# Optimization experiments

Measured on AMD Instinct MI355X. Metric: run time of the kernel, lower is better.

Reference implementation:

```python
import jax, jax.numpy as jnp
import numpy as np

B, L, C, H, W = 2, 3, 64, 32, 32
DI, N, DT_RANK, K = 128, 16, 4, 4  # d_inner=2*C, d_state, dt_rank=ceil(C/16), 4 scan dirs


def setup_inputs() -> dict:
    key = jax.random.key(0)
    ks = iter(jax.random.split(key, 48))
    nrm = lambda shape, s=0.02: jax.random.normal(next(ks), shape, jnp.float32) * s
    return {
        "image_sequence": jax.random.normal(next(ks), (B, L, C, H, W), jnp.float32),
        "difficult_zone": jax.random.normal(next(ks), (B, C, H, W), jnp.float32),
        "sigma": jax.random.uniform(next(ks), (B, C, H, W), jnp.float32),
        # LayerNorm2d applied to each frame
        "norm_g": jnp.ones((C,)), "norm_b": jnp.zeros((C,)),
        # ConvolutionalResBlock (in=3C -> out=C), GroupNorm(num_groups=1)
        "gn1_g": jnp.ones((3 * C,)), "gn1_b": jnp.zeros((3 * C,)),
        "conv1_w": nrm((C, 3 * C, 3, 3)), "conv1_b": jnp.zeros((C,)),
        "gn2_g": jnp.ones((C,)), "gn2_b": jnp.zeros((C,)),
        "conv2_w": nrm((C, C, 3, 3)), "conv2_b": jnp.zeros((C,)),
        "skip_w": nrm((C, 3 * C, 1, 1)), "skip_b": jnp.zeros((C,)),
        # VSSBlock pre-norms
        "ln1_g": jnp.ones((C,)), "ln1_b": jnp.zeros((C,)),
        "ln2_g": jnp.ones((C,)), "ln2_b": jnp.zeros((C,)),
        # SS2D
        "in_proj_w": nrm((2 * DI, C)),
        "dwconv_w": nrm((DI, 1, 3, 3)), "dwconv_b": jnp.zeros((DI,)),
        "x_proj_w": nrm((K, DT_RANK + 2 * N, DI)),
        "dt_proj_w": nrm((K, DI, DT_RANK), 0.1),
        "dt_proj_b": jnp.log(jnp.expm1(jnp.full((K, DI), 0.01, jnp.float32))),
        "A_logs": jnp.log(jnp.tile(jnp.arange(1, N + 1, dtype=jnp.float32), (K * DI, 1))),
        "Ds": jnp.ones((K * DI,)),
        "out_norm_g": jnp.ones((DI,)), "out_norm_b": jnp.zeros((DI,)),
        "out_proj_w": nrm((C, DI)),
        # Mlp (hidden = C)
        "fc1_w": nrm((C, C)), "fc1_b": jnp.zeros((C,)),
        "fc2_w": nrm((C, C)), "fc2_b": jnp.zeros((C,)),
    }


def _ln(x, g, b, eps=1e-5):  # layernorm over last axis
    m = x.mean(-1, keepdims=True)
    v = x.var(-1, keepdims=True)
    return (x - m) * jax.lax.rsqrt(v + eps) * g + b


def _ln2d(x, g, b, eps=1e-6):  # per-pixel channel layernorm, NCHW
    m = x.mean(1, keepdims=True)
    v = x.var(1, keepdims=True)
    return (x - m) * jax.lax.rsqrt(v + eps) * g[None, :, None, None] + b[None, :, None, None]


def _gn1(x, g, b, eps=1e-5):  # GroupNorm(num_groups=1), NCHW
    m = x.mean((1, 2, 3), keepdims=True)
    v = x.var((1, 2, 3), keepdims=True)
    return (x - m) * jax.lax.rsqrt(v + eps) * g[None, :, None, None] + b[None, :, None, None]


def _conv(x, w, b, pad):
    y = jax.lax.conv_general_dilated(x, w, (1, 1), [(pad, pad), (pad, pad)],
                                     dimension_numbers=("NCHW", "OIHW", "NCHW"))
    return y + b[None, :, None, None]


def _forward(image_sequence, difficult_zone, sigma, norm_g, norm_b, gn1_g, gn1_b,
             conv1_w, conv1_b, gn2_g, gn2_b, conv2_w, conv2_b, skip_w, skip_b,
             ln1_g, ln1_b, ln2_g, ln2_b, in_proj_w, dwconv_w, dwconv_b, x_proj_w,
             dt_proj_w, dt_proj_b, A_logs, Ds, out_norm_g, out_norm_b, out_proj_w,
             fc1_w, fc1_b, fc2_w, fc2_b):
    b, l, c, h, w = image_sequence.shape
    bl, L2 = b * l, h * w
    # fold frame loop into batch (identical math per frame in the torch loop)
    frames = _ln2d(image_sequence.reshape(bl, c, h, w), norm_g, norm_b)
    dz = jnp.broadcast_to(difficult_zone[:, None], (b, l, c, h, w)).reshape(bl, c, h, w)
    sg = jnp.broadcast_to(sigma[:, None], (b, l, c, h, w)).reshape(bl, c, h, w)
    x = jnp.concatenate([dz, frames, sg], axis=1)  # [bl, 3c, h, w]
    # channel compressor: pre-act conv res block
    hdn = _conv(jax.nn.silu(_gn1(x, gn1_g, gn1_b)), conv1_w, conv1_b, 1)
    hdn = _conv(jax.nn.silu(_gn1(hdn, gn2_g, gn2_b)), conv2_w, conv2_b, 1)
    x = hdn + _conv(x, skip_w, skip_b, 0)          # [bl, c, h, w]
    x = x.transpose(0, 2, 3, 1)                    # [bl, h, w, c]
    # --- VSSBlock (pre-norm): x = x + SS2D(LN(x)) ---
    xn = _ln(x, ln1_g, ln1_b)
    xz = xn @ in_proj_w.T                          # [bl,h,w,2*DI]
    xc, z = jnp.split(xz, 2, axis=-1)
    xc = xc.transpose(0, 3, 1, 2)                  # [bl, DI, h, w]
    xc = jax.lax.conv_general_dilated(xc, dwconv_w, (1, 1), [(1, 1), (1, 1)],
                                      dimension_numbers=("NCHW", "OIHW", "NCHW"),
                                      feature_group_count=DI) + dwconv_b[None, :, None, None]
    xc = jax.nn.silu(xc)
    # 4-direction scan inputs (HW, WH, and their reverses)
    xf = xc.reshape(bl, DI, L2)
    xt = xc.transpose(0, 1, 3, 2).reshape(bl, DI, L2)
    xs = jnp.stack([xf, xt], axis=1)
    xs = jnp.concatenate([xs, jnp.flip(xs, axis=-1)], axis=1)  # [bl, 4, DI, L2]
    x_dbl = jnp.einsum("bkdl,kcd->bkcl", xs, x_proj_w)
    dts, Bs, Cs = jnp.split(x_dbl, [DT_RANK, DT_RANK + N], axis=2)
    dts = jnp.einsum("bkrl,kdr->bkdl", dts, dt_proj_w) + dt_proj_b[None, :, :, None]
    dts = jax.nn.softplus(dts)                     # [bl, 4, DI, L2]
    A = -jnp.exp(A_logs).reshape(K, DI, N)
    dA = jnp.exp(dts[..., None] * A[None, :, :, None, :])            # [bl,4,DI,L2,N]
    dBu = dts[..., None] * Bs.transpose(0, 1, 3, 2)[:, :, None] * xs[..., None]
    a_t = dA.transpose(3, 0, 1, 2, 4)              # [L2, bl, 4, DI, N]
    bu_t = dBu.transpose(3, 0, 1, 2, 4)
    c_t = Cs.transpose(3, 0, 1, 2)                 # [L2, bl, 4, N]

    def step(hid, inp):
        a_i, bu_i, c_i = inp
        hid = a_i * hid + bu_i
        return hid, jnp.einsum("bkdn,bkn->bkd", hid, c_i)

    h0 = jnp.zeros((bl, K, DI, N), xs.dtype)
    _, ys = jax.lax.scan(step, h0, (a_t, bu_t, c_t))                 # [L2, bl, 4, DI]
    ys = ys.transpose(1, 2, 3, 0) + xs * Ds.reshape(K, DI)[None, :, :, None]
    inv = jnp.flip(ys[:, 2:4], axis=-1)
    y = (ys[:, 0] + inv[:, 0]
         + ys[:, 1].reshape(bl, DI, w, h).transpose(0, 1, 3, 2).reshape(bl, DI, L2)
         + inv[:, 1].reshape(bl, DI, w, h).transpose(0, 1, 3, 2).reshape(bl, DI, L2))
    y = _ln(y.transpose(0, 2, 1), out_norm_g, out_norm_b).reshape(bl, h, w, DI)
    y = y * jax.nn.silu(z)
    x = x + y @ out_proj_w.T
    # --- x = x + Mlp(LN(x)) ---
    xn = _ln(x, ln2_g, ln2_b)
    x = x + (jax.nn.gelu(xn @ fc1_w.T + fc1_b, approximate=False) @ fc2_w.T + fc2_b)
    return x.transpose(0, 3, 1, 2).reshape(b, l, c, h, w)


def reference(image_sequence, difficult_zone, sigma, norm_g, norm_b, gn1_g, gn1_b,
              conv1_w, conv1_b, gn2_g, gn2_b, conv2_w, conv2_b, skip_w, skip_b,
              ln1_g, ln1_b, ln2_g, ln2_b, in_proj_w, dwconv_w, dwconv_b, x_proj_w,
              dt_proj_w, dt_proj_b, A_logs, Ds, out_norm_g, out_norm_b, out_proj_w,
              fc1_w, fc1_b, fc2_w, fc2_b):
    return _forward(image_sequence, difficult_zone, sigma, norm_g, norm_b, gn1_g, gn1_b,
                    conv1_w, conv1_b, gn2_g, gn2_b, conv2_w, conv2_b, skip_w, skip_b,
                    ln1_g, ln1_b, ln2_g, ln2_b, in_proj_w, dwconv_w, dwconv_b, x_proj_w,
                    dt_proj_w, dt_proj_b, A_logs, Ds, out_norm_g, out_norm_b, out_proj_w,
                    fc1_w, fc1_b, fc2_w, fc2_b)
```

## Files before the change

### kernel.cpp

```cpp
#include <hip/hip_runtime.h>
#include <math.h>

#define BL    6
#define CCH   64
#define C3    192
#define L2    1024
#define DIC   128
#define NST   16
#define K4    4
#define PSTR  1088
#define NCH   32

#define LOG2E 1.44269504088896340736f
#define LN2C  0.69314718055994530942f

__device__ __forceinline__ float fexp(float x){ return __builtin_amdgcn_exp2f(x*LOG2E); }
__device__ __forceinline__ float fsilu(float x){ return x / (1.f + fexp(-x)); }
__device__ __forceinline__ float fsoftplus(float x){
  if (x > 20.f) return x;
  return __builtin_amdgcn_logf(1.f + fexp(x)) * LN2C;
}
__device__ __forceinline__ float fgelu(float x){
  return 0.5f*x*(1.f + erff(x*0.70710678118654752440f));
}

__global__ __launch_bounds__(256) void k_ln2d(const float* __restrict__ img,
    const float* __restrict__ dz, const float* __restrict__ sg,
    const float* __restrict__ g, const float* __restrict__ b, float* __restrict__ x3c,
    float* __restrict__ psum1, float* __restrict__ psq1){
  __shared__ float ps[4][64], pq[4][64];
  int s = blockIdx.x >> 4;
  int lane = threadIdx.x & 63;
  int cg = threadIdx.x >> 6;
  int p = ((blockIdx.x & 15) << 6) + lane;
  int bsmp = s/3;
  const float* fr = img + (size_t)s*CCH*L2;
  float vals[16]; float sm=0.f, sq=0.f;
  #pragma unroll
  for (int j=0;j<16;++j){
    int c = cg*16+j;
    float v = fr[c*L2+p];
    vals[j]=v; sm+=v; sq+=v*v;
  }
  ps[cg][lane]=sm; pq[cg][lane]=sq;
  __syncthreads();
  sm = ps[0][lane]+ps[1][lane]+ps[2][lane]+ps[3][lane];
  sq = pq[0][lane]+pq[1][lane]+pq[2][lane]+pq[3][lane];
  float mean = sm*(1.f/CCH); float var = sq*(1.f/CCH) - mean*mean;
  float rs = rsqrtf(var + 1e-6f);
  float* o = x3c + (size_t)s*C3*L2;
  const float* dzp = dz + (size_t)bsmp*CCH*L2;
  const float* sgp = sg + (size_t)bsmp*CCH*L2;
  float gsm=0.f, gsq=0.f;
  #pragma unroll
  for (int j=0;j<16;++j){
    int c = cg*16+j;
    float dzv = dzp[c*L2+p];
    float nv  = (vals[j]-mean)*rs*g[c] + b[c];
    float sgv = sgp[c*L2+p];
    o[c*L2+p] = dzv;
    o[(CCH+c)*L2+p] = nv;
    o[(2*CCH+c)*L2+p] = sgv;
    gsm += dzv+nv+sgv; gsq += dzv*dzv+nv*nv+sgv*sgv;
  }
  for (int m=1;m<64;m<<=1){ gsm+=__shfl_xor(gsm,m,64); gsq+=__shfl_xor(gsq,m,64); }
  __syncthreads();
  if (lane==0){ ps[cg][0]=gsm; pq[cg][0]=gsq; }
  __syncthreads();
  if (threadIdx.x==0){
    psum1[blockIdx.x] = ps[0][0]+ps[1][0]+ps[2][0]+ps[3][0];
    psq1 [blockIdx.x] = pq[0][0]+pq[1][0]+pq[2][0]+pq[3][0];
  }
}

__global__ __launch_bounds__(256) void k_gnact_pad(const float* __restrict__ x,
    const float* __restrict__ psum, const float* __restrict__ psq,
    const float* __restrict__ g, const float* __restrict__ b,
    int ch, int parts, float inv_n, float eps, float* __restrict__ out){
  int bx = blockIdx.x;
  int s = bx / ch; int c = bx % ch;
  int tid = threadIdx.x;
  float sm=0.f, sq=0.f;
  for (int i=0;i<parts;++i){ sm += psum[s*parts+i]; sq += psq[s*parts+i]; }
  float mean = sm*inv_n;
  float var = sq*inv_n - mean*mean;
  float rs = rsqrtf(var + eps);
  float gc = g[c]*rs; float bc = b[c] - mean*rs*g[c];
  float4 v = *(const float4*)(x + (size_t)bx*1024 + tid*4);
  float4 o; o.x = fsilu(v.x*gc+bc); o.y = fsilu(v.y*gc+bc);
  o.z = fsilu(v.z*gc+bc); o.w = fsilu(v.w*gc+bc);
  float* pl = out + (size_t)bx*PSTR;
  *(float4*)(pl + 32 + tid*4) = o;
  float4 z4 = make_float4(0.f,0.f,0.f,0.f);
  if (tid < 8)  *(float4*)(pl + tid*4) = z4;
  else if (tid < 16) *(float4*)(pl + 1056 + (tid-8)*4) = z4;
}

__device__ __forceinline__ void conv_row_acc(float4& a0, float4& a1, float4 mid, float lf, float rt,
    const float* wp0, const float* wp1){
  float w0=wp0[0], w1=wp0[1], w2=wp0[2];
  a0.x = fmaf(w0,lf,   fmaf(w1,mid.x, fmaf(w2,mid.y, a0.x)));
  a0.y = fmaf(w0,mid.x,fmaf(w1,mid.y, fmaf(w2,mid.z, a0.y)));
  a0.z = fmaf(w0,mid.y,fmaf(w1,mid.z, fmaf(w2,mid.w, a0.z)));
  a0.w = fmaf(w0,mid.z,fmaf(w1,mid.w, fmaf(w2,rt,    a0.w)));
  float v0=wp1[0], v1=wp1[1], v2=wp1[2];
  a1.x = fmaf(v0,lf,   fmaf(v1,mid.x, fmaf(v2,mid.y, a1.x)));
  a1.y = fmaf(v0,mid.x,fmaf(v1,mid.y, fmaf(v2,mid.z, a1.y)));
  a1.z = fmaf(v0,mid.y,fmaf(v1,mid.z, fmaf(v2,mid.w, a1.z)));
  a1.w = fmaf(v0,mid.z,fmaf(v1,mid.w, fmaf(v2,rt,    a1.w)));
}

__device__ __forceinline__ void conv_ci_body(float4 m0, float4 m1, float4 m2, int q,
    const float* wp0, const float* wp1, float4& a0, float4& a1){
  float lf0=__shfl_up(m0.w,1,64), rt0=__shfl_down(m0.x,1,64);
  float lf1=__shfl_up(m1.w,1,64), rt1=__shfl_down(m1.x,1,64);
  float lf2=__shfl_up(m2.w,1,64), rt2=__shfl_down(m2.x,1,64);
  if (q==0){ lf0=0.f; lf1=0.f; lf2=0.f; }
  if (q==7){ rt0=0.f; rt1=0.f; rt2=0.f; }
  conv_row_acc(a0,a1,m0,lf0,rt0, wp0+0, wp1+0);
  conv_row_acc(a0,a1,m1,lf1,rt1, wp0+3, wp1+3);
  conv_row_acc(a0,a1,m2,lf2,rt2, wp0+6, wp1+6);
}

__global__ __launch_bounds__(256) void k_conv1_split(const float* __restrict__ xact,
    const float* __restrict__ w, float* __restrict__ part){
  int bx = blockIdx.x; int kk = bx&7; int cop=(bx>>3)&31; int s=bx>>8;
  int co0 = cop*2, co1 = co0+1;
  int tid = threadIdx.x; int row = tid>>3; int q = tid&7; int col0 = q*4;
  float4 a0 = make_float4(0.f,0.f,0.f,0.f);
  float4 a1 = make_float4(0.f,0.f,0.f,0.f);
  int ci0 = kk*24;
  const float* pl = xact + ((size_t)s*C3 + ci0)*PSTR + row*32 + col0;
  const float* wp0 = w + (size_t)(co0*C3 + ci0)*9;
  const float* wp1 = w + (size_t)(co1*C3 + ci0)*9;
  float4 m0 = *(const float4*)(pl);
  float4 m1 = *(const float4*)(pl+32);
  float4 m2 = *(const float4*)(pl+64);
  #pragma unroll 2
  for (int i=0;i<24;++i){
    const float* pn = pl + (i<23 ? PSTR : 0);
    float4 n0 = *(const float4*)(pn);
    float4 n1 = *(const float4*)(pn+32);
    float4 n2 = *(const float4*)(pn+64);
    conv_ci_body(m0,m1,m2,q, wp0, wp1, a0, a1);
    wp0 += 9; wp1 += 9; pl = pn; m0=n0; m1=n1; m2=n2;
  }
  float* pp = part + (size_t)kk*(BL*CCH*L2) + ((size_t)s*CCH+co0)*L2 + row*32+col0;
  *(float4*)pp = a0;
  *(float4*)(pp+L2) = a1;
}

__global__ __launch_bounds__(256) void k_reduce1(const float* __restrict__ part,
    const float* __restrict__ bias, float* __restrict__ h1,
    float* __restrict__ psum2, float* __restrict__ psq2){
  int co = blockIdx.x & 63; int s = blockIdx.x >> 6;
  size_t ofs = ((size_t)s*CCH+co)*L2 + threadIdx.x*4;
  const size_t stride = (size_t)BL*CCH*L2;
  float4 acc = *(const float4*)(part + ofs);
  #pragma unroll
  for (int kk=1;kk<8;++kk){
    float4 r = *(const float4*)(part + (size_t)kk*stride + ofs);
    acc.x += r.x; acc.y += r.y; acc.z += r.z; acc.w += r.w;
  }
  float bv = bias[co];
  acc.x += bv; acc.y += bv; acc.z += bv; acc.w += bv;
  *(float4*)(h1 + ofs) = acc;
  float sm = acc.x+acc.y+acc.z+acc.w;
  float sq = acc.x*acc.x+acc.y*acc.y+acc.z*acc.z+acc.w*acc.w;
  for (int m=1;m<64;m<<=1){ sm+=__shfl_xor(sm,m,64); sq+=__shfl_xor(sq,m,64); }
  __shared__ float s_sm[4], s_sq[4];
  int wv = threadIdx.x>>6;
  if ((threadIdx.x&63)==0){ s_sm[wv]=sm; s_sq[wv]=sq; }
  __syncthreads();
  if (threadIdx.x==0){
    psum2[blockIdx.x] = s_sm[0]+s_sm[1]+s_sm[2]+s_sm[3];
    psq2 [blockIdx.x] = s_sq[0]+s_sq[1]+s_sq[2]+s_sq[3];
  }
}

__global__ __launch_bounds__(256) void k_conv2_split(const float* __restrict__ xact2,
    const float* __restrict__ x3c, const float* __restrict__ w2,
    const float* __restrict__ wsk, float* __restrict__ part){
  int t = blockIdx.x; int role = t % 3; t /= 3;
  int cop = t & 31; int s = t >> 5;
  int co0 = cop*2, co1 = co0+1;
  int tid = threadIdx.x; int row = tid>>3; int q = tid&7; int col0 = q*4;
  int p = row*32+col0;
  float4 a0 = make_float4(0.f,0.f,0.f,0.f);
  float4 a1 = make_float4(0.f,0.f,0.f,0.f);
  if (role < 2){
    int ci0 = role*32;
    const float* pl = xact2 + ((size_t)s*CCH + ci0)*PSTR + row*32 + col0;
    const float* wp0 = w2 + (size_t)(co0*CCH + ci0)*9;
    const float* wp1 = w2 + (size_t)(co1*CCH + ci0)*9;
    float4 m0 = *(const float4*)(pl);
    float4 m1 = *(const float4*)(pl+32);
    float4 m2 = *(const float4*)(pl+64);
    #pragma unroll 2
    for (int i=0;i<32;++i){
      const float* pn = pl + (i<31 ? PSTR : 0);
      float4 n0 = *(const float4*)(pn);
      float4 n1 = *(const float4*)(pn+32);
      float4 n2 = *(const float4*)(pn+64);
      conv_ci_body(m0,m1,m2,q, wp0, wp1, a0, a1);
      wp0 += 9; wp1 += 9; pl = pn; m0=n0; m1=n1; m2=n2;
    }
  } else {
    const float* x3 = x3c + (size_t)s*C3*L2 + p;
    #pragma unroll 4
    for (int ci=0; ci<C3; ++ci){
      float4 v = *(const float4*)(x3 + (size_t)ci*L2);
      float ws0 = wsk[co0*C3+ci], ws1 = wsk[co1*C3+ci];
      a0.x = fmaf(ws0,v.x,a0.x); a0.y = fmaf(ws0,v.y,a0.y); a0.z = fmaf(ws0,v.z,a0.z); a0.w = fmaf(ws0,v.w,a0.w);
      a1.x = fmaf(ws1,v.x,a1.x); a1.y = fmaf(ws1,v.y,a1.y); a1.z = fmaf(ws1,v.z,a1.z); a1.w = fmaf(ws1,v.w,a1.w);
    }
  }
  float* pp = part + (size_t)role*(BL*CCH*L2) + ((size_t)s*CCH+co0)*L2 + p;
  *(float4*)pp = a0;
  *(float4*)(pp+L2) = a1;
}

__global__ __launch_bounds__(256) void k_reduce2(const float* __restrict__ part,
    const float* __restrict__ b2, const float* __restrict__ bsk,
    float* __restrict__ xp, float* __restrict__ x_cmaj){
  int co = blockIdx.x & 63; int s = blockIdx.x >> 6;
  int p = threadIdx.x*4;
  size_t ofs = ((size_t)s*CCH+co)*L2 + p;
  const size_t stride = (size_t)BL*CCH*L2;
  float4 r0 = *(const float4*)(part + ofs);
  float4 r1 = *(const float4*)(part + stride + ofs);
  float4 r2 = *(const float4*)(part + 2*stride + ofs);
  float bv = b2[co]+bsk[co];
  float4 o;
  o.x = r0.x+r1.x+r2.x+bv;
  o.y = r0.y+r1.y+r2.y+bv;
  o.z = r0.z+r1.z+r2.z+bv;
  o.w = r0.w+r1.w+r2.w+bv;
  *(float4*)(x_cmaj + ofs) = o;
  float* xpb = xp + ((size_t)s*L2 + p)*CCH + co;
  xpb[0] = o.x; xpb[CCH] = o.y; xpb[2*CCH] = o.z; xpb[3*CCH] = o.w;
}

__global__ __launch_bounds__(256) void k_ln1_inproj(const float* __restrict__ xp,
    const float* __restrict__ g, const float* __restrict__ b, const float* __restrict__ W,
    float* __restrict__ xc, float* __restrict__ z_t){
  __shared__ float xn_s[64*65];
  int bx = blockIdx.x; int oq = bx & 3; int pg = (bx>>2)&15; int s = bx>>6;
  int p0 = pg*64;
  int tid = threadIdx.x; int wv = __builtin_amdgcn_readfirstlane(tid>>6); int lane = tid&63;
  for (int j=0;j<16;++j){
    int pl = wv*16 + j; int p = p0 + pl;
    float v = xp[((size_t)s*L2 + p)*CCH + lane];
    float sm = v, sq = v*v;
    for (int m=1;m<64;m<<=1){ sm += __shfl_xor(sm,m,64); sq += __shfl_xor(sq,m,64); }
    float mean = sm*(1.f/64.f); float var = sq*(1.f/64.f) - mean*mean;
    float rs = rsqrtf(var + 1e-5f);
    xn_s[pl*65 + lane] = (v-mean)*rs*g[lane] + b[lane];
  }
  __syncthreads();
  int px_l = tid & 63;
  int og = __builtin_amdgcn_readfirstlane(tid >> 6);
  int o0 = oq*64 + og*16;
  float acc[16];
  #pragma unroll
  for (int oi=0;oi<16;++oi) acc[oi]=0.f;
  for (int c=0;c<64;++c){
    float xv = xn_s[px_l*65 + c];
    #pragma unroll
    for (int oi=0;oi<16;++oi) acc[oi] = fmaf(W[(o0+oi)*64 + c], xv, acc[oi]);
  }
  int p = p0 + px_l;
  if (oq < 2){
    #pragma unroll
    for (int oi=0;oi<16;++oi) xc[((size_t)s*DIC + o0 + oi)*L2 + p] = acc[oi];
  } else {
    #pragma unroll
    for (int oi=0;oi<16;++oi) z_t[((size_t)s*DIC + (o0-128) + oi)*L2 + p] = acc[oi];
  }
}

__global__ __launch_bounds__(256) void k_dwconv(const float* __restrict__ xc,
    const float* __restrict__ w, const float* __restrict__ bias, float* __restrict__ xconv){
  int bx = blockIdx.x; int dch = bx & 127; int s = bx >> 7;
  int tid = threadIdx.x; int row = tid>>3; int q = tid&7; int col0 = q*4;
  const float* xr = xc + ((size_t)s*DIC+dch)*L2;
  const float* wp = w + dch*9;
  float bv = bias[dch];
  float4 acc = make_float4(bv,bv,bv,bv);
  #pragma unroll
  for (int dy=-1;dy<=1;++dy){
    int r = row+dy;
    float4 mid = make_float4(0.f,0.f,0.f,0.f);
    if (0<=r && r<32) mid = *(const float4*)(xr + r*32 + col0);
    float lf = __shfl_up(mid.w,1,64); if(q==0) lf=0.f;
    float rt = __shfl_down(mid.x,1,64); if(q==7) rt=0.f;
    float w0=wp[(dy+1)*3], w1=wp[(dy+1)*3+1], w2=wp[(dy+1)*3+2];
    acc.x = fmaf(w0,lf,   fmaf(w1,mid.x, fmaf(w2,mid.y, acc.x)));
    acc.y = fmaf(w0,mid.x,fmaf(w1,mid.y, fmaf(w2,mid.z, acc.y)));
    acc.z = fmaf(w0,mid.y,fmaf(w1,mid.z, fmaf(w2,mid.w, acc.z)));
    acc.w = fmaf(w0,mid.z,fmaf(w1,mid.w, fmaf(w2,rt,    acc.w)));
  }
  acc.x = fsilu(acc.x); acc.y = fsilu(acc.y); acc.z = fsilu(acc.z); acc.w = fsilu(acc.w);
  *(float4*)(xconv + ((size_t)s*DIC+dch)*L2 + row*32+col0) = acc;
}

__global__ __launch_bounds__(256) void k_xproj_dt(const float* __restrict__ xconv,
    const float* __restrict__ W, const float* __restrict__ dtw, const float* __restrict__ dtb,
    float* __restrict__ dtp, float* __restrict__ Bp, float* __restrict__ Cp,
    float* __restrict__ u_t){
  __shared__ float smem[128*68];
  int bx = blockIdx.x; int pg = bx & 15; int sk = bx >> 4;
  int k = sk & 3; int s = sk >> 2;
  int tid = threadIdx.x;
  for (int i = tid; i < 128*16; i += 256){
    int dr = i>>4; int j4 = (i&15)*4;
    float4 v = *(const float4*)(xconv + ((size_t)(s*DIC + dr))*L2 + pg*64 + j4);
    *(float4*)&smem[dr*68 + j4] = v;
  }
  __syncthreads();
  if (k == 0){
    float* ub = u_t + ((size_t)(s*L2) + pg*64)*DIC;
    for (int i = tid; i < 64*128; i += 256){
      int px2 = i>>7; int dd = i&127;
      ub[(size_t)px2*DIC + dd] = smem[dd*68 + px2];
    }
  }
  int px = tid & 63;
  int cgrp = __builtin_amdgcn_readfirstlane(tid >> 6);
  int c0 = cgrp*9;
  const float* wb = W + (size_t)(k*36 + c0)*DIC;
  float acc[9];
  #pragma unroll
  for (int ci=0;ci<9;++ci) acc[ci]=0.f;
  for (int d=0; d<DIC; ++d){
    float xv = smem[d*68 + px];
    #pragma unroll
    for (int ci=0;ci<9;++ci) acc[ci] = fmaf(wb[ci*DIC+d], xv, acc[ci]);
  }
  __syncthreads();
  #pragma unroll
  for (int ci=0;ci<9;++ci) smem[(c0+ci)*68 + px] = acc[ci];
  __syncthreads();
  int d = tid & 127; int half = tid >> 7;
  float w0 = dtw[(k*DIC+d)*4+0], w1 = dtw[(k*DIC+d)*4+1];
  float w2 = dtw[(k*DIC+d)*4+2], w3 = dtw[(k*DIC+d)*4+3];
  float bb = dtb[k*DIC+d];
  float* dout = dtp + ((size_t)sk*L2 + pg*64)*DIC + d;
  for (int pp = half*32; pp < half*32+32; ++pp){
    float r0 = smem[0*68+pp], r1 = smem[1*68+pp], r2 = smem[2*68+pp], r3 = smem[3*68+pp];
    float val = fsoftplus(fmaf(w0,r0,fmaf(w1,r1,fmaf(w2,r2,fmaf(w3,r3,bb)))));
    dout[(size_t)pp*DIC] = val;
  }
  float* Bb = Bp + ((size_t)sk*L2 + pg*64)*NST;
  float* Cb = Cp + ((size_t)sk*L2 + pg*64)*NST;
  for (int i = tid; i < 1024; i += 256){
    int pp = i>>4; int n = i&15;
    Bb[pp*NST + n] = smem[(4+n)*68 + pp];
    Cb[pp*NST + n] = smem[(20+n)*68 + pp];
  }
}

__device__ __forceinline__ int scan_pix32(int ch, int j, int k){
  if (k==0) return ch*32 + j;
  if (k==1) return j*32 + ch;
  if (k==2) return 1023 - (ch*32 + j);
  return 1023 - (j*32 + ch);
}

struct StepB { float dtv, uv; float4 B0,B1,B2,B3; };
__device__ __forceinline__ StepB loadB(const float* db, const float* ub, const float* Bb, int p){
  StepB r;
  r.dtv = db[(size_t)p*DIC]; r.uv = ub[(size_t)p*DIC];
  const float* bp = Bb + p*NST;
  r.B0 = *(const float4*)bp; r.B1 = *(const float4*)(bp+4);
  r.B2 = *(const float4*)(bp+8); r.B3 = *(const float4*)(bp+12);
  return r;
}

__global__ __launch_bounds__(256,2) void k_scan_part3(const float* __restrict__ dtp,
    const float* __restrict__ u_t, const float* __restrict__ Bp,
    const float* __restrict__ A_logs, float* __restrict__ hend, float* __restrict__ prodA){
  int bx = blockIdx.x; int chp = bx & 15; int sk = bx >> 4;
  int k = sk & 3; int s = sk >> 2;
  int tid = threadIdx.x; int d = tid & 127; int ch = chp*2 + (tid>>7);
  float aco[16];
  {
    const float* ab = A_logs + (size_t)(k*DIC+d)*NST;
    #pragma unroll
    for (int n=0;n<16;++n) aco[n] = -LOG2E * fexp(ab[n]);
  }
  float h[16], Pr[16];
  #pragma unroll
  for (int n=0;n<16;++n){ h[n]=0.f; Pr[n]=1.f; }
  const float* db = dtp + (size_t)sk*L2*DIC + d;
  const float* ub = u_t + (size_t)s*L2*DIC + d;
  const float* Bb = Bp + (size_t)sk*L2*NST;
  StepB cur = loadB(db, ub, Bb, scan_pix32(ch, 0, k));
  #pragma unroll 4
  for (int j=0;j<32;++j){
    StepB nxt;
    if (j < 31) nxt = loadB(db, ub, Bb, scan_pix32(ch, j+1, k));
    float tv = cur.dtv*cur.uv;
    #define PSTEP(NI, BV) { float a_ = __builtin_amdgcn_exp2f(cur.dtv*aco[NI]); \
      h[NI] = fmaf(a_, h[NI], tv*(BV)); Pr[NI] *= a_; }
    PSTEP(0,cur.B0.x) PSTEP(1,cur.B0.y) PSTEP(2,cur.B0.z) PSTEP(3,cur.B0.w)
    PSTEP(4,cur.B1.x) PSTEP(5,cur.B1.y) PSTEP(6,cur.B1.z) PSTEP(7,cur.B1.w)
    PSTEP(8,cur.B2.x) PSTEP(9,cur.B2.y) PSTEP(10,cur.B2.z) PSTEP(11,cur.B2.w)
    PSTEP(12,cur.B3.x) PSTEP(13,cur.B3.y) PSTEP(14,cur.B3.z) PSTEP(15,cur.B3.w)
    #undef PSTEP
    cur = nxt;
  }
  size_t base = ((size_t)(sk*NCH + ch)*DIC + d)*NST;
  #pragma unroll
  for (int q4=0;q4<4;++q4){
    *(float4*)(hend + base + q4*4)  = make_float4(h[q4*4],h[q4*4+1],h[q4*4+2],h[q4*4+3]);
    *(float4*)(prodA + base + q4*4) = make_float4(Pr[q4*4],Pr[q4*4+1],Pr[q4*4+2],Pr[q4*4+3]);
  }
}

__global__ __launch_bounds__(256) void k_scan_fix3(const float* __restrict__ hend,
    float* prodA_Hin){
  int t = blockIdx.x*256 + threadIdx.x;
  int n = t & 15; int d = (t>>4) & 127; int sk = t >> 11;
  float H = 0.f;
  for (int ch=0; ch<NCH; ++ch){
    size_t idx = ((size_t)(sk*NCH + ch)*DIC + d)*NST + n;
    float pa = prodA_Hin[idx];
    float he = hend[idx];
    prodA_Hin[idx] = H;
    H = fmaf(pa, H, he);
  }
}

__global__ __launch_bounds__(256,2) void k_scan_y3(const float* __restrict__ dtp,
    const float* __restrict__ u_t, const float* __restrict__ Bp, const float* __restrict__ Cp,
    const float* __restrict__ A_logs, const float* __restrict__ Ds,
    const float* __restrict__ Hin, float* __restrict__ ys_t){
  int bx = blockIdx.x; int chp = bx & 15; int sk = bx >> 4;
  int k = sk & 3; int s = sk >> 2;
  int tid = threadIdx.x; int d = tid & 127; int ch = chp*2 + (tid>>7);
  float aco[16];
  {
    const float* ab = A_logs + (size_t)(k*DIC+d)*NST;
    #pragma unroll
    for (int n=0;n<16;++n) aco[n] = -LOG2E * fexp(ab[n]);
  }
  float Dv = Ds[k*DIC+d];
  float h[16];
  size_t hbase = ((size_t)(sk*NCH + ch)*DIC + d)*NST;
  #pragma unroll
  for (int q4=0;q4<4;++q4){
    float4 hv = *(const float4*)(Hin + hbase + q4*4);
    h[q4*4]=hv.x; h[q4*4+1]=hv.y; h[q4*4+2]=hv.z; h[q4*4+3]=hv.w;
  }
  const float* db = dtp + (size_t)sk*L2*DIC + d;
  const float* ub = u_t + (size_t)s*L2*DIC + d;
  const float* Bb = Bp + (size_t)sk*L2*NST;
  const float* Cb = Cp + (size_t)sk*L2*NST;
  float* yb = ys_t + (size_t)sk*L2*DIC + d;
  int pcur = scan_pix32(ch, 0, k);
  StepB cur = loadB(db, ub, Bb, pcur);
  float4 Cc0 = *(const float4*)(Cb + pcur*NST);
  float4 Cc1 = *(const float4*)(Cb + pcur*NST + 4);
  float4 Cc2 = *(const float4*)(Cb + pcur*NST + 8);
  float4 Cc3 = *(const float4*)(Cb + pcur*NST + 12);
  #pragma unroll 4
  for (int j=0;j<32;++j){
    StepB nxt; float4 Cn0, Cn1, Cn2, Cn3; int pn = pcur;
    if (j < 31){
      pn = scan_pix32(ch, j+1, k);
      nxt = loadB(db, ub, Bb, pn);
      Cn0 = *(const float4*)(Cb + pn*NST);
      Cn1 = *(const float4*)(Cb + pn*NST + 4);
      Cn2 = *(const float4*)(Cb + pn*NST + 8);
      Cn3 = *(const float4*)(Cb + pn*NST + 12);
    }
    float tv = cur.dtv*cur.uv;
    float y0=0.f, y1=0.f, y2=0.f, y3=0.f;
    #define YSTEP(NI, BV, CV, YA) { float a_ = __builtin_amdgcn_exp2f(cur.dtv*aco[NI]); \
      h[NI] = fmaf(a_, h[NI], tv*(BV)); YA = fmaf(h[NI], (CV), YA); }
    YSTEP(0,cur.B0.x,Cc0.x,y0) YSTEP(1,cur.B0.y,Cc0.y,y1) YSTEP(2,cur.B0.z,Cc0.z,y2) YSTEP(3,cur.B0.w,Cc0.w,y3)
    YSTEP(4,cur.B1.x,Cc1.x,y0) YSTEP(5,cur.B1.y,Cc1.y,y1) YSTEP(6,cur.B1.z,Cc1.z,y2) YSTEP(7,cur.B1.w,Cc1.w,y3)
    YSTEP(8,cur.B2.x,Cc2.x,y0) YSTEP(9,cur.B2.y,Cc2.y,y1) YSTEP(10,cur.B2.z,Cc2.z,y2) YSTEP(11,cur.B2.w,Cc2.w,y3)
    YSTEP(12,cur.B3.x,Cc3.x,y0) YSTEP(13,cur.B3.y,Cc3.y,y1) YSTEP(14,cur.B3.z,Cc3.z,y2) YSTEP(15,cur.B3.w,Cc3.w,y3)
    #undef YSTEP
    yb[(size_t)pcur*DIC] = fmaf(cur.uv, Dv, (y0+y1)+(y2+y3));
    cur = nxt; Cc0 = Cn0; Cc1 = Cn1; Cc2 = Cn2; Cc3 = Cn3; pcur = pn;
  }
}

__global__ __launch_bounds__(256) void k_tail(const float* __restrict__ ys_t,
    const float* __restrict__ z_t, const float* __restrict__ ong, const float* __restrict__ onb,
    const float* __restrict__ Wop, const float* __restrict__ x_cmaj,
    const float* __restrict__ g2, const float* __restrict__ b2n,
    const float* __restrict__ w1, const float* __restrict__ b1,
    const float* __restrict__ w2, const float* __restrict__ b2,
    float* __restrict__ out){
  __shared__ float yt[128*17];
  __shared__ float xvt[64*17];
  __shared__ float ts[64*17];
  int s = blockIdx.x >> 6; int pg = blockIdx.x & 63;
  int tid = threadIdx.x;
  {
    int wv = __builtin_amdgcn_readfirstlane(tid>>6); int lane = tid&63;
    int d0 = lane, d1 = lane+64;
    for (int i=0;i<4;++i){
      int px = i*4 + wv; int p = pg*16 + px;
      const float* yb = ys_t + ((size_t)(s*4)*L2 + p)*DIC;
      float ya = yb[d0] + yb[(size_t)L2*DIC + d0] + yb[(size_t)2*L2*DIC + d0] + yb[(size_t)3*L2*DIC + d0];
      float yc = yb[d1] + yb[(size_t)L2*DIC + d1] + yb[(size_t)2*L2*DIC + d1] + yb[(size_t)3*L2*DIC + d1];
      float sm = ya+yc, sq = ya*ya+yc*yc;
      for (int m=1;m<64;m<<=1){ sm+=__shfl_xor(sm,m,64); sq+=__shfl_xor(sq,m,64); }
      float mean = sm*(1.f/128.f); float var = sq*(1.f/128.f)-mean*mean;
      float rs = rsqrtf(var + 1e-5f);
      float yn0 = (ya-mean)*rs*ong[d0] + onb[d0];
      float yn1 = (yc-mean)*rs*ong[d1] + onb[d1];
      float zv0 = z_t[((size_t)s*DIC+d0)*L2 + p];
      float zv1 = z_t[((size_t)s*DIC+d1)*L2 + p];
      yt[d0*17 + px] = yn0 * fsilu(zv0);
      yt[d1*17 + px] = yn1 * fsilu(zv1);
    }
  }
  __syncthreads();
  {
    int px = tid & 15; int cgp = tid >> 4;
    int c0 = cgp*4;
    float a0=0.f,a1=0.f,a2=0.f,a3=0.f;
    for (int d=0; d<DIC; ++d){
      float yv = yt[d*17 + px];
      a0 = fmaf(Wop[(c0+0)*DIC + d], yv, a0);
      a1 = fmaf(Wop[(c0+1)*DIC + d], yv, a1);
      a2 = fmaf(Wop[(c0+2)*DIC + d], yv, a2);
      a3 = fmaf(Wop[(c0+3)*DIC + d], yv, a3);
    }
    int p = pg*16 + px;
    size_t base = ((size_t)s*CCH + c0)*L2 + p;
    xvt[(c0+0)*17 + px] = x_cmaj[base]      + a0;
    xvt[(c0+1)*17 + px] = x_cmaj[base+L2]   + a1;
    xvt[(c0+2)*17 + px] = x_cmaj[base+2*L2] + a2;
    xvt[(c0+3)*17 + px] = x_cmaj[base+3*L2] + a3;
  }
  __syncthreads();
  int px = tid & 15; int cgp = tid >> 4;
  float sm=0.f, sq=0.f;
  for (int c=0;c<64;++c){ float v = xvt[c*17+px]; sm+=v; sq+=v*v; }
  float mean = sm*(1.f/64.f);
  float rs = rsqrtf(sq*(1.f/64.f) - mean*mean + 1e-5f);
  int o0 = cgp*4;
  float t[4];
  #pragma unroll
  for (int oi=0;oi<4;++oi) t[oi] = b1[o0+oi];
  for (int c=0;c<64;++c){
    float xn = (xvt[c*17+px]-mean)*rs*g2[c] + b2n[c];
    #pragma unroll
    for (int oi=0;oi<4;++oi) t[oi] = fmaf(xn, w1[(o0+oi)*64 + c], t[oi]);
  }
  #pragma unroll
  for (int oi=0;oi<4;++oi) ts[(o0+oi)*17 + px] = fgelu(t[oi]);
  __syncthreads();
  int c0 = cgp*4;
  float acc[4];
  #pragma unroll
  for (int ci=0;ci<4;++ci) acc[ci] = xvt[(c0+ci)*17+px] + b2[c0+ci];
  for (int o=0;o<64;++o){
    float tv = ts[o*17+px];
    #pragma unroll
    for (int ci=0;ci<4;++ci) acc[ci] = fmaf(tv, w2[(c0+ci)*64 + o], acc[ci]);
  }
  int p = pg*16 + px;
  #pragma unroll
  for (int ci=0;ci<4;++ci) out[((size_t)s*CCH + c0+ci)*L2 + p] = acc[ci];
}

extern "C" void kernel_launch(void* const* d_in, const int* in_sizes, int n_in,
                              void* d_out, int out_size, void* d_ws, size_t ws_size,
                              hipStream_t stream){
  (void)in_sizes; (void)n_in; (void)out_size; (void)ws_size;
  const float* img      = (const float*)d_in[0];
  const float* dz       = (const float*)d_in[1];
  const float* sg       = (const float*)d_in[2];
  const float* norm_g   = (const float*)d_in[3];
  const float* norm_b   = (const float*)d_in[4];
  const float* gn1_g    = (const float*)d_in[5];
  const float* gn1_b    = (const float*)d_in[6];
  const float* conv1_w  = (const float*)d_in[7];
  const float* conv1_b  = (const float*)d_in[8];
  const float* gn2_g    = (const float*)d_in[9];
  const float* gn2_b    = (const float*)d_in[10];
  const float* conv2_w  = (const float*)d_in[11];
  const float* conv2_b  = (const float*)d_in[12];
  const float* skip_w   = (const float*)d_in[13];
  const float* skip_b   = (const float*)d_in[14];
  const float* ln1_g    = (const float*)d_in[15];
  const float* ln1_b    = (const float*)d_in[16];
  const float* ln2_g    = (const float*)d_in[17];
  const float* ln2_b    = (const float*)d_in[18];
  const float* in_proj_w= (const float*)d_in[19];
  const float* dwconv_w = (const float*)d_in[20];
  const float* dwconv_b = (const float*)d_in[21];
  const float* x_proj_w = (const float*)d_in[22];
  const float* dt_proj_w= (const float*)d_in[23];
  const float* dt_proj_b= (const float*)d_in[24];
  const float* A_logs   = (const float*)d_in[25];
  const float* Ds       = (const float*)d_in[26];
  const float* out_norm_g = (const float*)d_in[27];
  const float* out_norm_b = (const float*)d_in[28];
  const float* out_proj_w = (const float*)d_in[29];
  const float* fc1_w    = (const float*)d_in[30];
  const float* fc1_b    = (const float*)d_in[31];
  const float* fc2_w    = (const float*)d_in[32];
  const float* fc2_b    = (const float*)d_in[33];

  float* ws = (float*)d_ws;
  float* x3c    = ws;
  float* xact1  = x3c    + 1179648;
  float* h1     = xact1  + 1253376;
  float* xact2  = h1     + 393216;
  float* xp     = xact2  + 417792;
  float* x_cmaj = xp     + 393216;
  float* z_t    = x_cmaj + 393216;
  float* xc     = z_t    + 786432;
  float* xconv  = xc     + 786432;
  float* hole   = xconv  + 786432;
  float* dtp    = hole   + 884736;
  float* ys_t   = dtp    + 3145728;
  float* statsb = ys_t   + 3145728;
  float* psum1  = statsb;
  float* psq1   = statsb + 96;
  float* psum2  = statsb + 192;
  float* psq2   = statsb + 576;
  float* part1  = dtp;
  float* part2  = ys_t;
  float* hend   = x3c;
  float* prodA  = xconv;
  float* u_t    = h1;
  float* Bp     = xp;
  float* Cp     = xc;

  k_ln2d<<<96, 256, 0, stream>>>(img, dz, sg, norm_g, norm_b, x3c, psum1, psq1);
  k_gnact_pad<<<6*C3, 256, 0, stream>>>(x3c, psum1, psq1, gn1_g, gn1_b, C3, 16,
                                        1.f/(C3*L2), 1e-5f, xact1);
  k_conv1_split<<<1536, 256, 0, stream>>>(xact1, conv1_w, part1);
  k_reduce1<<<384, 256, 0, stream>>>(part1, conv1_b, h1, psum2, psq2);
  k_gnact_pad<<<6*CCH, 256, 0, stream>>>(h1, psum2, psq2, gn2_g, gn2_b, CCH, 64,
                                         1.f/(CCH*L2), 1e-5f, xact2);
  k_conv2_split<<<576, 256, 0, stream>>>(xact2, x3c, conv2_w, skip_w, part2);
  k_reduce2<<<384, 256, 0, stream>>>(part2, conv2_b, skip_b, xp, x_cmaj);
  k_ln1_inproj<<<384, 256, 0, stream>>>(xp, ln1_g, ln1_b, in_proj_w, xc, z_t);
  k_dwconv<<<768, 256, 0, stream>>>(xc, dwconv_w, dwconv_b, xconv);
  k_xproj_dt<<<384, 256, 0, stream>>>(xconv, x_proj_w, dt_proj_w, dt_proj_b, dtp, Bp, Cp, u_t);
  k_scan_part3<<<384, 256, 0, stream>>>(dtp, u_t, Bp, A_logs, hend, prodA);
  k_scan_fix3<<<192, 256, 0, stream>>>(hend, prodA);
  k_scan_y3<<<384, 256, 0, stream>>>(dtp, u_t, Bp, Cp, A_logs, Ds, prodA, ys_t);
  k_tail<<<384, 256, 0, stream>>>(ys_t, z_t, out_norm_g, out_norm_b, out_proj_w, x_cmaj,
                                  ln2_g, ln2_b, fc1_w, fc1_b, fc2_w, fc2_b, (float*)d_out);
}
```

Before: 305.4 us.

## Recompute dt inside scans, replace chunk prodA with dt sum, widen ln2d grid

The scan no longer reads a materialized per-channel dt tensor. xproj now writes only the 4 low-rank dt values per pixel, and both scan kernels recompute softplus(dt_proj) inline. Instead of storing 16 cumulative decay products per chunk, part3 stores the chunk sum of dt, and fix3 rebuilds the product as exp2(A·sum). This cuts large intermediate traffic at the cost of extra ALU work in the scans. Separately, k_ln2d is split across 4x more blocks, with 16 pixels per block, to raise parallelism, which changes the stats partition count.

Result: no change. 304.7 us (-0.3%).

```diff
diff --git a/kernel.cpp b/kernel.cpp
--- a/kernel.cpp
+++ b/kernel.cpp
@@ -28,33 +28,37 @@
     const float* __restrict__ dz, const float* __restrict__ sg,
     const float* __restrict__ g, const float* __restrict__ b, float* __restrict__ x3c,
     float* __restrict__ psum1, float* __restrict__ psq1){
-  __shared__ float ps[4][64], pq[4][64];
-  int s = blockIdx.x >> 4;
-  int lane = threadIdx.x & 63;
-  int cg = threadIdx.x >> 6;
-  int p = ((blockIdx.x & 15) << 6) + lane;
+  __shared__ float ps[4][16], pq[4][16], gs[4], gq[4];
+  int s = blockIdx.x >> 6;
+  int pg = blockIdx.x & 63;
+  int tid = threadIdx.x;
+  int px = tid & 15; int cg = tid >> 4;
+  int wv = tid >> 6; int lane = tid & 63;
+  int p = pg*16 + px;
   int bsmp = s/3;
   const float* fr = img + (size_t)s*CCH*L2;
-  float vals[16]; float sm=0.f, sq=0.f;
-  #pragma unroll
-  for (int j=0;j<16;++j){
-    int c = cg*16+j;
-    float v = fr[c*L2+p];
+  float vals[4]; float sm=0.f, sq=0.f;
+  #pragma unroll
+  for (int j=0;j<4;++j){
+    int c = cg*4 + j;
+    float v = fr[c*L2 + p];
     vals[j]=v; sm+=v; sq+=v*v;
   }
-  ps[cg][lane]=sm; pq[cg][lane]=sq;
-  __syncthreads();
-  sm = ps[0][lane]+ps[1][lane]+ps[2][lane]+ps[3][lane];
-  sq = pq[0][lane]+pq[1][lane]+pq[2][lane]+pq[3][lane];
-  float mean = sm*(1.f/CCH); float var = sq*(1.f/CCH) - mean*mean;
+  sm += __shfl_xor(sm,16,64); sq += __shfl_xor(sq,16,64);
+  sm += __shfl_xor(sm,32,64); sq += __shfl_xor(sq,32,64);
+  if (lane < 16){ ps[wv][lane]=sm; pq[wv][lane]=sq; }
+  __syncthreads();
+  sm = ps[0][px]+ps[1][px]+ps[2][px]+ps[3][px];
+  sq = pq[0][px]+pq[1][px]+pq[2][px]+pq[3][px];
+  float mean = sm*(1.f/CCH); float var = sq*(1.f/CCH)-mean*mean;
   float rs = rsqrtf(var + 1e-6f);
   float* o = x3c + (size_t)s*C3*L2;
   const float* dzp = dz + (size_t)bsmp*CCH*L2;
   const float* sgp = sg + (size_t)bsmp*CCH*L2;
   float gsm=0.f, gsq=0.f;
   #pragma unroll
-  for (int j=0;j<16;++j){
-    int c = cg*16+j;
+  for (int j=0;j<4;++j){
+    int c = cg*4+j;
     float dzv = dzp[c*L2+p];
     float nv  = (vals[j]-mean)*rs*g[c] + b[c];
     float sgv = sgp[c*L2+p];
@@ -64,12 +68,11 @@
     gsm += dzv+nv+sgv; gsq += dzv*dzv+nv*nv+sgv*sgv;
   }
   for (int m=1;m<64;m<<=1){ gsm+=__shfl_xor(gsm,m,64); gsq+=__shfl_xor(gsq,m,64); }
-  __syncthreads();
-  if (lane==0){ ps[cg][0]=gsm; pq[cg][0]=gsq; }
-  __syncthreads();
-  if (threadIdx.x==0){
-    psum1[blockIdx.x] = ps[0][0]+ps[1][0]+ps[2][0]+ps[3][0];
-    psq1 [blockIdx.x] = pq[0][0]+pq[1][0]+pq[2][0]+pq[3][0];
+  if (lane==0){ gs[wv]=gsm; gq[wv]=gsq; }
+  __syncthreads();
+  if (tid==0){
+    psum1[blockIdx.x] = gs[0]+gs[1]+gs[2]+gs[3];
+    psq1 [blockIdx.x] = gq[0]+gq[1]+gq[2]+gq[3];
   }
 }
 
@@ -305,8 +308,8 @@
 }
 
 __global__ __launch_bounds__(256) void k_xproj_dt(const float* __restrict__ xconv,
-    const float* __restrict__ W, const float* __restrict__ dtw, const float* __restrict__ dtb,
-    float* __restrict__ dtp, float* __restrict__ Bp, float* __restrict__ Cp,
+    const float* __restrict__ W,
+    float* __restrict__ dtr, float* __restrict__ Bp, float* __restrict__ Cp,
     float* __restrict__ u_t){
   __shared__ float smem[128*68];
   int bx = blockIdx.x; int pg = bx & 15; int sk = bx >> 4;
@@ -341,15 +344,9 @@
   #pragma unroll
   for (int ci=0;ci<9;++ci) smem[(c0+ci)*68 + px] = acc[ci];
   __syncthreads();
-  int d = tid & 127; int half = tid >> 7;
-  float w0 = dtw[(k*DIC+d)*4+0], w1 = dtw[(k*DIC+d)*4+1];
-  float w2 = dtw[(k*DIC+d)*4+2], w3 = dtw[(k*DIC+d)*4+3];
-  float bb = dtb[k*DIC+d];
-  float* dout = dtp + ((size_t)sk*L2 + pg*64)*DIC + d;
-  for (int pp = half*32; pp < half*32+32; ++pp){
-    float r0 = smem[0*68+pp], r1 = smem[1*68+pp], r2 = smem[2*68+pp], r3 = smem[3*68+pp];
-    float val = fsoftplus(fmaf(w0,r0,fmaf(w1,r1,fmaf(w2,r2,fmaf(w3,r3,bb)))));
-    dout[(size_t)pp*DIC] = val;
+  {
+    int pp = tid >> 2; int r = tid & 3;
+    dtr[((size_t)sk*L2 + pg*64 + pp)*4 + r] = smem[r*68 + pp];
   }
   float* Bb = Bp + ((size_t)sk*L2 + pg*64)*NST;
   float* Cb = Cp + ((size_t)sk*L2 + pg*64)*NST;
@@ -367,19 +364,24 @@
   return 1023 - (j*32 + ch);
 }
 
-struct StepB { float dtv, uv; float4 B0,B1,B2,B3; };
-__device__ __forceinline__ StepB loadB(const float* db, const float* ub, const float* Bb, int p){
+struct StepB { float4 dt4; float uv; float4 B0,B1,B2,B3; };
+__device__ __forceinline__ StepB loadB(const float* dr, const float* ub, const float* Bb, int p){
   StepB r;
-  r.dtv = db[(size_t)p*DIC]; r.uv = ub[(size_t)p*DIC];
+  r.dt4 = *(const float4*)(dr + (size_t)p*4);
+  r.uv = ub[(size_t)p*DIC];
   const float* bp = Bb + p*NST;
   r.B0 = *(const float4*)bp; r.B1 = *(const float4*)(bp+4);
   r.B2 = *(const float4*)(bp+8); r.B3 = *(const float4*)(bp+12);
   return r;
 }
-
-__global__ __launch_bounds__(256,2) void k_scan_part3(const float* __restrict__ dtp,
+__device__ __forceinline__ float dt_eval(float4 w4, float bb, float4 d4){
+  return fsoftplus(fmaf(w4.x,d4.x,fmaf(w4.y,d4.y,fmaf(w4.z,d4.z,fmaf(w4.w,d4.w,bb)))));
+}
+
+__global__ __launch_bounds__(256,2) void k_scan_part3(const float* __restrict__ dtr,
+    const float* __restrict__ dtw, const float* __restrict__ dtb,
     const float* __restrict__ u_t, const float* __restrict__ Bp,
-    const float* __restrict__ A_logs, float* __restrict__ hend, float* __restrict__ prodA){
+    const float* __restrict__ A_logs, float* __restrict__ hend, float* __restrict__ Ssum){
   int bx = blockIdx.x; int chp = bx & 15; int sk = bx >> 4;
   int k = sk & 3; int s = sk >> 2;
   int tid = threadIdx.x; int d = tid & 127; int ch = chp*2 + (tid>>7);
@@ -389,20 +391,24 @@
     #pragma unroll
     for (int n=0;n<16;++n) aco[n] = -LOG2E * fexp(ab[n]);
   }
-  float h[16], Pr[16];
-  #pragma unroll
-  for (int n=0;n<16;++n){ h[n]=0.f; Pr[n]=1.f; }
-  const float* db = dtp + (size_t)sk*L2*DIC + d;
+  float4 w4 = *(const float4*)(dtw + (size_t)(k*DIC+d)*4);
+  float bb = dtb[k*DIC+d];
+  float h[16]; float Sacc = 0.f;
+  #pragma unroll
+  for (int n=0;n<16;++n) h[n]=0.f;
+  const float* dr = dtr + (size_t)sk*L2*4;
   const float* ub = u_t + (size_t)s*L2*DIC + d;
   const float* Bb = Bp + (size_t)sk*L2*NST;
-  StepB cur = loadB(db, ub, Bb, scan_pix32(ch, 0, k));
+  StepB cur = loadB(dr, ub, Bb, scan_pix32(ch, 0, k));
   #pragma unroll 4
   for (int j=0;j<32;++j){
     StepB nxt;
-    if (j < 31) nxt = loadB(db, ub, Bb, scan_pix32(ch, j+1, k));
-    float tv = cur.dtv*cur.uv;
-    #define PSTEP(NI, BV) { float a_ = __builtin_amdgcn_exp2f(cur.dtv*aco[NI]); \
-      h[NI] = fmaf(a_, h[NI], tv*(BV)); Pr[NI] *= a_; }
+    if (j < 31) nxt = loadB(dr, ub, Bb, scan_pix32(ch, j+1, k));
+    float dtv = dt_eval(w4, bb, cur.dt4);
+    Sacc += dtv;
+    float tv = dtv*cur.uv;
+    #define PSTEP(NI, BV) { float a_ = __builtin_amdgcn_exp2f(dtv*aco[NI]); \
+      h[NI] = fmaf(a_, h[NI], tv*(BV)); }
     PSTEP(0,cur.B0.x) PSTEP(1,cur.B0.y) PSTEP(2,cur.B0.z) PSTEP(3,cur.B0.w)
     PSTEP(4,cur.B1.x) PSTEP(5,cur.B1.y) PSTEP(6,cur.B1.z) PSTEP(7,cur.B1.w)
     PSTEP(8,cur.B2.x) PSTEP(9,cur.B2.y) PSTEP(10,cur.B2.z) PSTEP(11,cur.B2.w)
@@ -412,27 +418,30 @@
   }
   size_t base = ((size_t)(sk*NCH + ch)*DIC + d)*NST;
   #pragma unroll
-  for (int q4=0;q4<4;++q4){
+  for (int q4=0;q4<4;++q4)
     *(float4*)(hend + base + q4*4)  = make_float4(h[q4*4],h[q4*4+1],h[q4*4+2],h[q4*4+3]);
-    *(float4*)(prodA + base + q4*4) = make_float4(Pr[q4*4],Pr[q4*4+1],Pr[q4*4+2],Pr[q4*4+3]);
-  }
+  Ssum[(size_t)(sk*NCH + ch)*DIC + d] = Sacc;
 }
 
 __global__ __launch_bounds__(256) void k_scan_fix3(const float* __restrict__ hend,
-    float* prodA_Hin){
+    const float* __restrict__ Ssum, const float* __restrict__ A_logs,
+    float* __restrict__ Hin){
   int t = blockIdx.x*256 + threadIdx.x;
-  int n = t & 15; int d = (t>>4) & 127; int sk = t >> 11;
+  int n = t & 15; int d = (t>>4) & 127; int sk = t >> 11; int k = sk & 3;
+  float aco = -LOG2E * fexp(A_logs[(size_t)(k*DIC+d)*NST + n]);
   float H = 0.f;
+  #pragma unroll 8
   for (int ch=0; ch<NCH; ++ch){
-    size_t idx = ((size_t)(sk*NCH + ch)*DIC + d)*NST + n;
-    float pa = prodA_Hin[idx];
-    float he = hend[idx];
-    prodA_Hin[idx] = H;
+    size_t sidx = (size_t)(sk*NCH + ch)*DIC + d;
+    float pa = __builtin_amdgcn_exp2f(aco * Ssum[sidx]);
+    float he = hend[sidx*NST + n];
+    Hin[sidx*NST + n] = H;
     H = fmaf(pa, H, he);
   }
 }
 
-__global__ __launch_bounds__(256,2) void k_scan_y3(const float* __restrict__ dtp,
+__global__ __launch_bounds__(256,2) void k_scan_y3(const float* __restrict__ dtr,
+    const float* __restrict__ dtw, const float* __restrict__ dtb,
     const float* __restrict__ u_t, const float* __restrict__ Bp, const float* __restrict__ Cp,
     const float* __restrict__ A_logs, const float* __restrict__ Ds,
     const float* __restrict__ Hin, float* __restrict__ ys_t){
@@ -445,6 +454,8 @@
     #pragma unroll
     for (int n=0;n<16;++n) aco[n] = -LOG2E * fexp(ab[n]);
   }
+  float4 w4 = *(const float4*)(dtw + (size_t)(k*DIC+d)*4);
+  float bb = dtb[k*DIC+d];
   float Dv = Ds[k*DIC+d];
   float h[16];
   size_t hbase = ((size_t)(sk*NCH + ch)*DIC + d)*NST;
@@ -453,13 +464,13 @@
     float4 hv = *(const float4*)(Hin + hbase + q4*4);
     h[q4*4]=hv.x; h[q4*4+1]=hv.y; h[q4*4+2]=hv.z; h[q4*4+3]=hv.w;
   }
-  const float* db = dtp + (size_t)sk*L2*DIC + d;
+  const float* dr = dtr + (size_t)sk*L2*4;
   const float* ub = u_t + (size_t)s*L2*DIC + d;
   const float* Bb = Bp + (size_t)sk*L2*NST;
   const float* Cb = Cp + (size_t)sk*L2*NST;
   float* yb = ys_t + (size_t)sk*L2*DIC + d;
   int pcur = scan_pix32(ch, 0, k);
-  StepB cur = loadB(db, ub, Bb, pcur);
+  StepB cur = loadB(dr, ub, Bb, pcur);
   float4 Cc0 = *(const float4*)(Cb + pcur*NST);
   float4 Cc1 = *(const float4*)(Cb + pcur*NST + 4);
   float4 Cc2 = *(const float4*)(Cb + pcur*NST + 8);
@@ -469,15 +480,16 @@
     StepB nxt; float4 Cn0, Cn1, Cn2, Cn3; int pn = pcur;
     if (j < 31){
       pn = scan_pix32(ch, j+1, k);
-      nxt = loadB(db, ub, Bb, pn);
+      nxt = loadB(dr, ub, Bb, pn);
       Cn0 = *(const float4*)(Cb + pn*NST);
       Cn1 = *(const float4*)(Cb + pn*NST + 4);
       Cn2 = *(const float4*)(Cb + pn*NST + 8);
       Cn3 = *(const float4*)(Cb + pn*NST + 12);
     }
-    float tv = cur.dtv*cur.uv;
+    float dtv = dt_eval(w4, bb, cur.dt4);
+    float tv = dtv*cur.uv;
     float y0=0.f, y1=0.f, y2=0.f, y3=0.f;
-    #define YSTEP(NI, BV, CV, YA) { float a_ = __builtin_amdgcn_exp2f(cur.dtv*aco[NI]); \
+    #define YSTEP(NI, BV, CV, YA) { float a_ = __builtin_amdgcn_exp2f(dtv*aco[NI]); \
       h[NI] = fmaf(a_, h[NI], tv*(BV)); YA = fmaf(h[NI], (CV), YA); }
     YSTEP(0,cur.B0.x,Cc0.x,y0) YSTEP(1,cur.B0.y,Cc0.y,y1) YSTEP(2,cur.B0.z,Cc0.z,y2) YSTEP(3,cur.B0.w,Cc0.w,y3)
     YSTEP(4,cur.B1.x,Cc1.x,y0) YSTEP(5,cur.B1.y,Cc1.y,y1) YSTEP(6,cur.B1.z,Cc1.z,y2) YSTEP(7,cur.B1.w,Cc1.w,y3)
@@ -622,23 +634,25 @@
   float* xc     = z_t    + 786432;
   float* xconv  = xc     + 786432;
   float* hole   = xconv  + 786432;
-  float* dtp    = hole   + 884736;
-  float* ys_t   = dtp    + 3145728;
+  float* scanbuf= hole   + 884736;
+  float* ys_t   = scanbuf+ 3145728;
   float* statsb = ys_t   + 3145728;
   float* psum1  = statsb;
-  float* psq1   = statsb + 96;
-  float* psum2  = statsb + 192;
-  float* psq2   = statsb + 576;
-  float* part1  = dtp;
+  float* psq1   = statsb + 384;
+  float* psum2  = statsb + 768;
+  float* psq2   = statsb + 1152;
+  float* part1  = scanbuf;
   float* part2  = ys_t;
   float* hend   = x3c;
-  float* prodA  = xconv;
   float* u_t    = h1;
   float* Bp     = xp;
   float* Cp     = xc;
-
-  k_ln2d<<<96, 256, 0, stream>>>(img, dz, sg, norm_g, norm_b, x3c, psum1, psq1);
-  k_gnact_pad<<<6*C3, 256, 0, stream>>>(x3c, psum1, psq1, gn1_g, gn1_b, C3, 16,
+  float* dtr    = hole;
+  float* Ssum   = hole + 98304;
+  float* Hin    = scanbuf;
+
+  k_ln2d<<<384, 256, 0, stream>>>(img, dz, sg, norm_g, norm_b, x3c, psum1, psq1);
+  k_gnact_pad<<<6*C3, 256, 0, stream>>>(x3c, psum1, psq1, gn1_g, gn1_b, C3, 64,
                                         1.f/(C3*L2), 1e-5f, xact1);
   k_conv1_split<<<1536, 256, 0, stream>>>(xact1, conv1_w, part1);
   k_reduce1<<<384, 256, 0, stream>>>(part1, conv1_b, h1, psum2, psq2);
@@ -648,10 +662,10 @@
   k_reduce2<<<384, 256, 0, stream>>>(part2, conv2_b, skip_b, xp, x_cmaj);
   k_ln1_inproj<<<384, 256, 0, stream>>>(xp, ln1_g, ln1_b, in_proj_w, xc, z_t);
   k_dwconv<<<768, 256, 0, stream>>>(xc, dwconv_w, dwconv_b, xconv);
-  k_xproj_dt<<<384, 256, 0, stream>>>(xconv, x_proj_w, dt_proj_w, dt_proj_b, dtp, Bp, Cp, u_t);
-  k_scan_part3<<<384, 256, 0, stream>>>(dtp, u_t, Bp, A_logs, hend, prodA);
-  k_scan_fix3<<<192, 256, 0, stream>>>(hend, prodA);
-  k_scan_y3<<<384, 256, 0, stream>>>(dtp, u_t, Bp, Cp, A_logs, Ds, prodA, ys_t);
+  k_xproj_dt<<<384, 256, 0, stream>>>(xconv, x_proj_w, dtr, Bp, Cp, u_t);
+  k_scan_part3<<<384, 256, 0, stream>>>(dtr, dt_proj_w, dt_proj_b, u_t, Bp, A_logs, hend, Ssum);
+  k_scan_fix3<<<192, 256, 0, stream>>>(hend, Ssum, A_logs, Hin);
+  k_scan_y3<<<384, 256, 0, stream>>>(dtr, dt_proj_w, dt_proj_b, u_t, Bp, Cp, A_logs, Ds, Hin, ys_t);
   k_tail<<<384, 256, 0, stream>>>(ys_t, z_t, out_norm_g, out_norm_b, out_proj_w, x_cmaj,
                                   ln2_g, ln2_b, fc1_w, fc1_b, fc2_w, fc2_b, (float*)d_out);
 }
```
